# Optimization experiments

Hardware: AMD Instinct MI355X
Metric: run time of the kernel (lower is better)

## Reference

```python
import jax, jax.numpy as jnp
import numpy as np


def gcn_conv(x, src, dst, W, b, n_nodes):
    """PyG-style GCNConv: add self-loops, symmetric deg^-1/2 normalization,
    linear transform, scatter-add aggregation to dst, then bias."""
    loop = jnp.arange(n_nodes, dtype=src.dtype)
    s = jnp.concatenate([src, loop])
    d = jnp.concatenate([dst, loop])
    deg = jax.ops.segment_sum(jnp.ones_like(d, x.dtype), d, num_segments=n_nodes)
    dinv = jax.lax.rsqrt(deg)  # deg >= 1 due to self-loops
    norm = dinv[s] * dinv[d]  # [E+N]
    h = x @ W.T  # [N, out]
    msg = h[s] * norm[:, None]  # [E+N, out]
    return jax.ops.segment_sum(msg, d, num_segments=n_nodes) + b


def setup_inputs() -> dict:
    key = jax.random.key(0)
    k = jax.random.split(key, 6)
    N, E, IN, HID, OUT = 100000, 1600000, 128, 128, 64
    x = jax.random.normal(k[0], (N, IN), dtype=jnp.float32)
    edge_index = jax.random.randint(k[1], (2, E), 0, N, dtype=jnp.int64)
    W1 = jax.random.normal(k[2], (HID, IN), dtype=jnp.float32) * 0.05
    b1 = jnp.zeros((HID,), dtype=jnp.float32)
    W2 = jax.random.normal(k[3], (OUT, HID), dtype=jnp.float32) * 0.05
    b2 = jnp.zeros((OUT,), dtype=jnp.float32)
    return {"x": x, "W1": W1, "b1": b1, "W2": W2, "b2": b2, "edge_index": edge_index}


def reference(x, W1, b1, W2, b2, edge_index):
    n_nodes = x.shape[0]
    src, dst = edge_index[0], edge_index[1]
    h = jax.nn.relu(gcn_conv(x, src, dst, W1, b1, n_nodes))
    return gcn_conv(h, src, dst, W2, b2, n_nodes)
```

## Files before the change

### kernel.cpp

```cpp
#include <hip/hip_runtime.h>
#include <hip/hip_bf16.h>


#define IN_F  128
#define HID_F 128
#define OUT_F 64

#define NPB     512
#define MAXBKT  256
#define CHUNK   4096
#define SLAB    12288
#define CAP     12288

typedef __bf16 bf16_t;
typedef __bf16 bf16x4 __attribute__((ext_vector_type(4)));
typedef __bf16 bf16x8 __attribute__((ext_vector_type(8)));
typedef float  f32x2  __attribute__((ext_vector_type(2)));
typedef float  f32x4  __attribute__((ext_vector_type(4)));
typedef unsigned u32x2 __attribute__((ext_vector_type(2)));
typedef unsigned u32x4 __attribute__((ext_vector_type(4)));

__global__ __launch_bounds__(256) void k_pre(const float* __restrict__ W1s,
                                             const float* __restrict__ W2s,
                                             bf16_t* __restrict__ Wdst,
                                             int n1, int n2,
                                             int* __restrict__ bcur, int nb16) {
    int i = blockIdx.x * 256 + threadIdx.x;
    if (i < n1) Wdst[i] = (bf16_t)W1s[i];
    else if (i < n1 + n2) Wdst[i] = (bf16_t)W2s[i - n1];
    if (blockIdx.x == gridDim.x - 1) {
        for (int j = threadIdx.x; j < nb16; j += 256) bcur[j] = 0;
    }
}

__global__ __launch_bounds__(256) void k_part(const int* __restrict__ src,
                                              const int* __restrict__ dst, int E,
                                              int* __restrict__ bcur,
                                              unsigned* __restrict__ part, int NBKT) {
    __shared__ int cnt[MAXBKT];
    __shared__ int base[MAXBKT];
    __shared__ int cstart[MAXBKT];
    __shared__ unsigned stg[CHUNK];
    __shared__ unsigned short sbk[CHUNK];
    int t = threadIdx.x;
    cnt[t] = 0;
    __syncthreads();
    int cbase = blockIdx.x * CHUNK;
    int cend = min(cbase + CHUNK, E);
    int clen = cend - cbase;
    for (int e = cbase + t; e < cend; e += 256)
        atomicAdd(&cnt[dst[e] >> 9], 1);
    __syncthreads();
    int c = cnt[t];
    cstart[t] = c;
    __syncthreads();
    for (int ofs = 1; ofs < 256; ofs <<= 1) {
        int add = (t >= ofs) ? cstart[t - ofs] : 0;
        __syncthreads();
        cstart[t] += add;
        __syncthreads();
    }
    int excl = cstart[t] - c;
    __syncthreads();
    cstart[t] = excl;
    base[t] = (c && t < NBKT) ? (t * SLAB + atomicAdd(&bcur[t * 16], c)) : 0;
    cnt[t] = 0;
    __syncthreads();
    for (int e = cbase + t; e < cend; e += 256) {
        int d = dst[e];
        int b = d >> 9;
        int lp = atomicAdd(&cnt[b], 1);
        int pos = cstart[b] + lp;
        stg[pos] = (unsigned)src[e] | ((unsigned)(d & 511) << 17);
        sbk[pos] = (unsigned short)b;
    }
    __syncthreads();
    for (int i = t; i < clen; i += 256) {
        int b = sbk[i];
        part[base[b] + (i - cstart[b])] = stg[i];
    }
}

__global__ __launch_bounds__(512) void k_bucket(const unsigned* __restrict__ part,
                                                const int* __restrict__ bcur,
                                                int2* __restrict__ off2,
                                                int* __restrict__ col,
                                                float* __restrict__ dinv, int N) {
    __shared__ int lcnt[NPB];
    __shared__ int lexc[NPB];
    __shared__ int lcur[NPB];
    __shared__ int psum[NPB];
    __shared__ int stage[CAP];
    int b = blockIdx.x;
    int t = threadIdx.x;
    int node0 = b * NPB;
    int e0s = b * SLAB;
    int cnt = bcur[b * 16];
    lcnt[t] = 0;
    __syncthreads();
    for (int i = t; i < cnt; i += 512)
        atomicAdd(&lcnt[part[e0s + i] >> 17], 1);
    __syncthreads();
    int pc = (lcnt[t] + 7) & ~7;
    psum[t] = pc;
    __syncthreads();
    for (int ofs = 1; ofs < NPB; ofs <<= 1) {
        int add = (t >= ofs) ? psum[t - ofs] : 0;
        __syncthreads();
        psum[t] += add;
        __syncthreads();
    }
    int run = psum[t] - pc;
    lexc[t] = run;
    lcur[t] = run;
    int node = node0 + t;
    if (node < N) {
        off2[node] = make_int2(e0s + run, e0s + run + pc);
        dinv[node] = rsqrtf((float)lcnt[t] + 1.0f);
    }
    __syncthreads();
    for (int i = t; i < cnt; i += 512) {
        unsigned p = part[e0s + i];
        int dl = p >> 17;
        int sv = (int)(p & 0x1FFFF);
        int lp = atomicAdd(&lcur[dl], 1);
        if (lp < CAP) stage[lp] = sv;
        else col[e0s + lp] = sv;
    }
    __syncthreads();
    {
        int en = lexc[t] + pc;
        for (int i = lcur[t]; i < en; i++) {
            if (i < CAP) stage[i] = N; else col[e0s + i] = N;
        }
    }
    __syncthreads();
    int tot = psum[NPB - 1];
    for (int i = t; i < tot && i < CAP; i += 512) col[e0s + i] = stage[i];
}

template <int NCOL, typename TIN>
__global__ __launch_bounds__(256) void k_gemm_mfma(const TIN* __restrict__ X,
                                                   const bf16_t* __restrict__ W,
                                                   const float* __restrict__ scale,
                                                   bf16_t* __restrict__ H, int N) {
    constexpr int CT = NCOL / 16;
    int wv = threadIdx.x >> 6, lane = threadIdx.x & 63;
    int quad = lane >> 4, l16 = lane & 15;
    int row0 = blockIdx.x * 128 + wv * 32;
    f32x4 acc[2][CT] = {};
#pragma unroll
    for (int ks = 0; ks < 4; ks++) {
        int k0 = ks * 32 + quad * 8;
        bf16x8 a[2];
#pragma unroll
        for (int rt = 0; rt < 2; rt++) {
            int r = row0 + rt * 16 + l16;
            if (r >= N) r = N - 1;
            const TIN* p = X + (size_t)r * 128 + k0;
            if constexpr (sizeof(TIN) == 4) {
                f32x4 x0 = *(const f32x4*)p;
                f32x4 x1 = *(const f32x4*)(p + 4);
                bf16x8 tt;
                tt[0] = (bf16_t)x0[0]; tt[1] = (bf16_t)x0[1];
                tt[2] = (bf16_t)x0[2]; tt[3] = (bf16_t)x0[3];
                tt[4] = (bf16_t)x1[0]; tt[5] = (bf16_t)x1[1];
                tt[6] = (bf16_t)x1[2]; tt[7] = (bf16_t)x1[3];
                a[rt] = tt;
            } else {
                a[rt] = *(const bf16x8*)p;
            }
        }
#pragma unroll
        for (int ct = 0; ct < CT; ct++) {
            bf16x8 bfrag = *(const bf16x8*)(W + (size_t)(ct * 16 + l16) * 128 + k0);
#pragma unroll
            for (int rt = 0; rt < 2; rt++)
                acc[rt][ct] = __builtin_amdgcn_mfma_f32_16x16x32_bf16(a[rt], bfrag, acc[rt][ct], 0, 0, 0);
        }
    }
#pragma unroll
    for (int rt = 0; rt < 2; rt++)
#pragma unroll
        for (int r4 = 0; r4 < 4; r4++) {
            int r = row0 + rt * 16 + quad * 4 + r4;
            if (r < N) {
                float sc = scale[r];
#pragma unroll
                for (int ct = 0; ct < CT; ct++)
                    H[(size_t)r * NCOL + ct * 16 + l16] = (bf16_t)(sc * acc[rt][ct][r4]);
            } else if (r == N) {
#pragma unroll
                for (int ct = 0; ct < CT; ct++)
                    H[(size_t)N * NCOL + ct * 16 + l16] = (bf16_t)0.f;
            }
        }
}

template <int ROWE>
__device__ __forceinline__ void gather8(const bf16_t* __restrict__ hp,
                                        const int* __restrict__ col, int e,
                                        u32x4* w) {
    int4 c0 = *(const int4*)(col + e);
    int4 c1 = *(const int4*)(col + e + 4);
    w[0] = *(const u32x4*)(hp + (unsigned)c0.x * (unsigned)ROWE);
    w[1] = *(const u32x4*)(hp + (unsigned)c0.y * (unsigned)ROWE);
    w[2] = *(const u32x4*)(hp + (unsigned)c0.z * (unsigned)ROWE);
    w[3] = *(const u32x4*)(hp + (unsigned)c0.w * (unsigned)ROWE);
    w[4] = *(const u32x4*)(hp + (unsigned)c1.x * (unsigned)ROWE);
    w[5] = *(const u32x4*)(hp + (unsigned)c1.y * (unsigned)ROWE);
    w[6] = *(const u32x4*)(hp + (unsigned)c1.z * (unsigned)ROWE);
    w[7] = *(const u32x4*)(hp + (unsigned)c1.w * (unsigned)ROWE);
}

__device__ __forceinline__ void accum8(const u32x4* w, f32x2* a2) {
#pragma unroll
    for (int u = 0; u < 8; u++)
#pragma unroll
        for (int k = 0; k < 4; k++) {
            f32x2 v;
            v.x = __uint_as_float(w[u][k] << 16);
            v.y = __uint_as_float(w[u][k] & 0xffff0000u);
            a2[k] += v;
        }
}

__global__ __launch_bounds__(256) void k_agg_gemm(const bf16_t* __restrict__ h,
                                                  const int2* __restrict__ off2,
                                                  const int* __restrict__ col,
                                                  const float* __restrict__ dinv,
                                                  const float* __restrict__ bias,
                                                  const bf16_t* __restrict__ W2,
                                                  bf16_t* __restrict__ h2, int N) {
    __shared__ float hl[16][132];
    __shared__ float dl[16];
    int lane = threadIdx.x & 63;
    int wv = threadIdx.x >> 6;
    int g = lane >> 4, fl = lane & 15;
    int node0 = blockIdx.x * 16;
    int node = node0 + wv * 4 + g;
    bool alive = node < N;
    int f = fl * 8;
    const bf16_t* hp = h + f;
    f32x2 a2[4] = {};
    float di = 0.f;
    if (alive) {
        u32x4 ws = *(const u32x4*)(hp + (unsigned)node * 128u);
        int2 oe = off2[node];
        di = dinv[node];
#pragma unroll
        for (int k = 0; k < 4; k++) {
            f32x2 v;
            v.x = __uint_as_float(ws[k] << 16);
            v.y = __uint_as_float(ws[k] & 0xffff0000u);
            a2[k] = v;
        }
        u32x4 w[8];
        for (int e = oe.x; e < oe.y; e += 8) {
            gather8<128>(hp, col, e, w);
            accum8(w, a2);
        }
    }
    f32x4 b0 = *(const f32x4*)(bias + f);
    f32x4 b1 = *(const f32x4*)(bias + f + 4);
    int lr = wv * 4 + g;
#pragma unroll
    for (int j = 0; j < 8; j++) {
        float bv = (j < 4) ? b0[j] : b1[j - 4];
        float val = a2[j >> 1][j & 1] * di + bv;
        hl[lr][f + j] = fmaxf(val, 0.f);
    }
    if (fl == 0) dl[lr] = di;
    __syncthreads();

    int quad = lane >> 4, l16 = lane & 15;
    f32x4 c4 = {0.f, 0.f, 0.f, 0.f};
#pragma unroll
    for (int ks = 0; ks < 4; ks++) {
        int k0 = ks * 32 + quad * 8;
        bf16x8 afr;
#pragma unroll
        for (int j = 0; j < 8; j++) afr[j] = (bf16_t)hl[l16][k0 + j];
        bf16x8 bfr = *(const bf16x8*)(W2 + (size_t)(wv * 16 + l16) * 128 + k0);
        c4 = __builtin_amdgcn_mfma_f32_16x16x32_bf16(afr, bfr, c4, 0, 0, 0);
    }
#pragma unroll
    for (int r4 = 0; r4 < 4; r4++) {
        int rr = quad * 4 + r4;
        int gn = node0 + rr;
        if (gn < N)
            h2[(size_t)gn * 64 + wv * 16 + l16] = (bf16_t)(dl[rr] * c4[r4]);
    }
    if (blockIdx.x == 0 && threadIdx.x < 32)
        ((unsigned*)h2)[(size_t)N * 32 + threadIdx.x] = 0u;
}

template <int ROWE, int LPN, bool RELU, typename TOUT>
__global__ __launch_bounds__(256) void k_agg(const bf16_t* __restrict__ h,
                                             const int2* __restrict__ off2,
                                             const int* __restrict__ col,
                                             const float* __restrict__ dinv,
                                             const float* __restrict__ bias,
                                             TOUT* __restrict__ out, int N) {
    constexpr int NPW = 64 / LPN;
    int lane = threadIdx.x & 63;
    int wv = threadIdx.x >> 6;
    int g = lane / LPN, fl = lane % LPN;
    int node = blockIdx.x * (4 * NPW) + wv * NPW + g;
    if (node >= N) return;
    int f = fl * 8;
    const bf16_t* hp = h + f;
    u32x4 ws = *(const u32x4*)(hp + (unsigned)node * (unsigned)ROWE);
    int2 oe = off2[node];
    float di = dinv[node];
    f32x2 a2[4];
#pragma unroll
    for (int k = 0; k < 4; k++) {
        f32x2 v;
        v.x = __uint_as_float(ws[k] << 16);
        v.y = __uint_as_float(ws[k] & 0xffff0000u);
        a2[k] = v;
    }
    u32x4 w[8];
    for (int e = oe.x; e < oe.y; e += 8) {
        gather8<ROWE>(hp, col, e, w);
        accum8(w, a2);
    }
    f32x4 b0 = *(const f32x4*)(bias + f);
    f32x4 b1 = *(const f32x4*)(bias + f + 4);
    float r[8];
#pragma unroll
    for (int j = 0; j < 8; j++) {
        float bv = (j < 4) ? b0[j] : b1[j - 4];
        float val = a2[j >> 1][j & 1] * di + bv;
        if (RELU) val = fmaxf(val, 0.f);
        r[j] = val;
    }
    if constexpr (sizeof(TOUT) == 2) {
        bf16x8 v;
#pragma unroll
        for (int j = 0; j < 8; j++) v[j] = (bf16_t)r[j];
        *(bf16x8*)((bf16_t*)out + (size_t)node * ROWE + f) = v;
    } else {
        f32x4 v0 = {r[0], r[1], r[2], r[3]};
        f32x4 v1 = {r[4], r[5], r[6], r[7]};
        *(f32x4*)((float*)out + (size_t)node * ROWE + f) = v0;
        *(f32x4*)((float*)out + (size_t)node * ROWE + f + 4) = v1;
    }
}

extern "C" void kernel_launch(void* const* d_in, const int* in_sizes, int n_in,
                              void* d_out, int out_size, void* d_ws, size_t ws_size,
                              hipStream_t stream) {
    const float* x  = (const float*)d_in[0];
    const float* W1 = (const float*)d_in[1];
    const float* b1 = (const float*)d_in[2];
    const float* W2 = (const float*)d_in[3];
    const float* b2 = (const float*)d_in[4];
    const int*   ei = (const int*)d_in[5];

    int N = in_sizes[0] / IN_F;
    int E = in_sizes[5] / 2;
    const int* src = ei;
    const int* dst = ei + E;
    int NBKT = (N + NPB - 1) / NPB;
    int pchunks = (E + CHUNK - 1) / CHUNK;

    size_t woff = 0;
    auto alloc = [&](size_t bytes) {
        void* p = (char*)d_ws + woff;
        woff += (bytes + 255) & ~(size_t)255;
        return p;
    };
    int*      bcur  = (int*)alloc((size_t)NBKT * 16 * 4);
    unsigned* part  = (unsigned*)alloc((size_t)NBKT * SLAB * 4);
    int*      col   = (int*)alloc((size_t)NBKT * SLAB * 4);
    int2*     off2  = (int2*)alloc((size_t)N * 8);
    float*    dinv  = (float*)alloc((size_t)N * 4);
    bf16_t*   Wb    = (bf16_t*)alloc((size_t)(HID_F * IN_F + OUT_F * HID_F) * 2);
    bf16_t*   W1b   = Wb;
    bf16_t*   W2b   = Wb + HID_F * IN_F;
    bf16_t*   h1    = (bf16_t*)alloc((size_t)(N + 1) * HID_F * 2);
    bf16_t*   h2b   = (bf16_t*)alloc((size_t)(N + 1) * OUT_F * 2);
    float*    outp  = (float*)d_out;

    int n1 = HID_F * IN_F, n2 = OUT_F * HID_F;
    int preblocks = (n1 + n2) / 256 + 1;
    k_pre<<<preblocks, 256, 0, stream>>>(W1, W2, Wb, n1, n2, bcur, NBKT * 16);
    k_part<<<pchunks, 256, 0, stream>>>(src, dst, E, bcur, part, NBKT);
    k_bucket<<<NBKT, 512, 0, stream>>>(part, bcur, off2, col, dinv, N);

    int gemm_blocks = (N + 127) / 128;

    k_gemm_mfma<HID_F, float><<<gemm_blocks, 256, 0, stream>>>(x, W1b, dinv, h1, N);
    k_agg_gemm<<<(N + 15) / 16, 256, 0, stream>>>(h1, off2, col, dinv, b1, W2b, h2b, N);
    k_agg<OUT_F, 8, false, float><<<(N + 31) / 32, 256, 0, stream>>>(h2b, off2, col, dinv, b2, outp, N);
}
```

Baseline: 251.9 us.

## Merge preprocessing kernels, compute degrees via global atomics, overlap GEMM with bucketing

The weight conversion now runs inside the partition kernel as extra blocks. The partition kernel also counts in-degrees with global atomics, so the first GEMM no longer waits for per-bucket CSR construction. The GEMM is launched as extra blocks of the bucket kernel so the two run side by side, and bucket entries are kept in registers between the counting and scatter passes. The aim is fewer launches and less serial dependency, paid for with 1.6M global atomics on deg, a memset, and rsqrt recomputed in each consumer.

```diff
diff --git a/kernel.cpp b/kernel.cpp
--- a/kernel.cpp
+++ b/kernel.cpp
@@ -11,45 +11,46 @@
 #define CHUNK   4096
 #define SLAB    12288
 #define CAP     12288
+#define KREG    20
 
 typedef __bf16 bf16_t;
-typedef __bf16 bf16x4 __attribute__((ext_vector_type(4)));
 typedef __bf16 bf16x8 __attribute__((ext_vector_type(8)));
 typedef float  f32x2  __attribute__((ext_vector_type(2)));
 typedef float  f32x4  __attribute__((ext_vector_type(4)));
-typedef unsigned u32x2 __attribute__((ext_vector_type(2)));
 typedef unsigned u32x4 __attribute__((ext_vector_type(4)));
 
-__global__ __launch_bounds__(256) void k_pre(const float* __restrict__ W1s,
-                                             const float* __restrict__ W2s,
-                                             bf16_t* __restrict__ Wdst,
-                                             int n1, int n2,
-                                             int* __restrict__ bcur, int nb16) {
-    int i = blockIdx.x * 256 + threadIdx.x;
-    if (i < n1) Wdst[i] = (bf16_t)W1s[i];
-    else if (i < n1 + n2) Wdst[i] = (bf16_t)W2s[i - n1];
-    if (blockIdx.x == gridDim.x - 1) {
-        for (int j = threadIdx.x; j < nb16; j += 256) bcur[j] = 0;
-    }
-}
-
-__global__ __launch_bounds__(256) void k_part(const int* __restrict__ src,
-                                              const int* __restrict__ dst, int E,
-                                              int* __restrict__ bcur,
-                                              unsigned* __restrict__ part, int NBKT) {
+__global__ __launch_bounds__(256) void k_setup(const int* __restrict__ src,
+                                               const int* __restrict__ dst, int E,
+                                               int* __restrict__ bcur,
+                                               unsigned* __restrict__ part,
+                                               int* __restrict__ deg,
+                                               const float* __restrict__ W1s,
+                                               const float* __restrict__ W2s,
+                                               bf16_t* __restrict__ Wdst,
+                                               int n1, int n2,
+                                               int NBKT, int pchunks) {
+    int t = threadIdx.x;
+    if ((int)blockIdx.x >= pchunks) {
+        int i = (blockIdx.x - pchunks) * 256 + t;
+        if (i < n1) Wdst[i] = (bf16_t)W1s[i];
+        else if (i < n1 + n2) Wdst[i] = (bf16_t)W2s[i - n1];
+        return;
+    }
     __shared__ int cnt[MAXBKT];
     __shared__ int base[MAXBKT];
     __shared__ int cstart[MAXBKT];
     __shared__ unsigned stg[CHUNK];
     __shared__ unsigned short sbk[CHUNK];
-    int t = threadIdx.x;
     cnt[t] = 0;
     __syncthreads();
     int cbase = blockIdx.x * CHUNK;
     int cend = min(cbase + CHUNK, E);
     int clen = cend - cbase;
-    for (int e = cbase + t; e < cend; e += 256)
-        atomicAdd(&cnt[dst[e] >> 9], 1);
+    for (int e = cbase + t; e < cend; e += 256) {
+        int d = dst[e];
+        atomicAdd(&cnt[d >> 9], 1);
+        atomicAdd(&deg[d], 1);
+    }
     __syncthreads();
     int c = cnt[t];
     cstart[t] = c;
@@ -81,84 +82,36 @@
     }
 }
 
-__global__ __launch_bounds__(512) void k_bucket(const unsigned* __restrict__ part,
-                                                const int* __restrict__ bcur,
-                                                int2* __restrict__ off2,
-                                                int* __restrict__ col,
-                                                float* __restrict__ dinv, int N) {
+__global__ __launch_bounds__(512) void k_mega2(const unsigned* __restrict__ part,
+                                               const int* __restrict__ bcur,
+                                               int2* __restrict__ off2,
+                                               int* __restrict__ col,
+                                               const int* __restrict__ deg,
+                                               const float* __restrict__ X,
+                                               const bf16_t* __restrict__ W1,
+                                               bf16_t* __restrict__ H,
+                                               int N, int NBKT) {
     __shared__ int lcnt[NPB];
     __shared__ int lexc[NPB];
     __shared__ int lcur[NPB];
     __shared__ int psum[NPB];
     __shared__ int stage[CAP];
-    int b = blockIdx.x;
     int t = threadIdx.x;
-    int node0 = b * NPB;
-    int e0s = b * SLAB;
-    int cnt = bcur[b * 16];
-    lcnt[t] = 0;
-    __syncthreads();
-    for (int i = t; i < cnt; i += 512)
-        atomicAdd(&lcnt[part[e0s + i] >> 17], 1);
-    __syncthreads();
-    int pc = (lcnt[t] + 7) & ~7;
-    psum[t] = pc;
-    __syncthreads();
-    for (int ofs = 1; ofs < NPB; ofs <<= 1) {
-        int add = (t >= ofs) ? psum[t - ofs] : 0;
-        __syncthreads();
-        psum[t] += add;
-        __syncthreads();
-    }
-    int run = psum[t] - pc;
-    lexc[t] = run;
-    lcur[t] = run;
-    int node = node0 + t;
-    if (node < N) {
-        off2[node] = make_int2(e0s + run, e0s + run + pc);
-        dinv[node] = rsqrtf((float)lcnt[t] + 1.0f);
-    }
-    __syncthreads();
-    for (int i = t; i < cnt; i += 512) {
-        unsigned p = part[e0s + i];
-        int dl = p >> 17;
-        int sv = (int)(p & 0x1FFFF);
-        int lp = atomicAdd(&lcur[dl], 1);
-        if (lp < CAP) stage[lp] = sv;
-        else col[e0s + lp] = sv;
-    }
-    __syncthreads();
-    {
-        int en = lexc[t] + pc;
-        for (int i = lcur[t]; i < en; i++) {
-            if (i < CAP) stage[i] = N; else col[e0s + i] = N;
-        }
-    }
-    __syncthreads();
-    int tot = psum[NPB - 1];
-    for (int i = t; i < tot && i < CAP; i += 512) col[e0s + i] = stage[i];
-}
-
-template <int NCOL, typename TIN>
-__global__ __launch_bounds__(256) void k_gemm_mfma(const TIN* __restrict__ X,
-                                                   const bf16_t* __restrict__ W,
-                                                   const float* __restrict__ scale,
-                                                   bf16_t* __restrict__ H, int N) {
-    constexpr int CT = NCOL / 16;
-    int wv = threadIdx.x >> 6, lane = threadIdx.x & 63;
-    int quad = lane >> 4, l16 = lane & 15;
-    int row0 = blockIdx.x * 128 + wv * 32;
-    f32x4 acc[2][CT] = {};
-#pragma unroll
-    for (int ks = 0; ks < 4; ks++) {
-        int k0 = ks * 32 + quad * 8;
-        bf16x8 a[2];
-#pragma unroll
-        for (int rt = 0; rt < 2; rt++) {
-            int r = row0 + rt * 16 + l16;
-            if (r >= N) r = N - 1;
-            const TIN* p = X + (size_t)r * 128 + k0;
-            if constexpr (sizeof(TIN) == 4) {
+    if ((int)blockIdx.x >= NBKT) {
+        int gb = blockIdx.x - NBKT;
+        int wv = t >> 6, lane = t & 63;
+        int quad = lane >> 4, l16 = lane & 15;
+        int row0 = gb * 256 + wv * 32;
+        f32x4 acc[2][8] = {};
+#pragma unroll
+        for (int ks = 0; ks < 4; ks++) {
+            int k0 = ks * 32 + quad * 8;
+            bf16x8 a[2];
+#pragma unroll
+            for (int rt = 0; rt < 2; rt++) {
+                int r = row0 + rt * 16 + l16;
+                if (r >= N) r = N - 1;
+                const float* p = X + (size_t)r * 128 + k0;
                 f32x4 x0 = *(const f32x4*)p;
                 f32x4 x1 = *(const f32x4*)(p + 4);
                 bf16x8 tt;
@@ -167,34 +120,98 @@
                 tt[4] = (bf16_t)x1[0]; tt[5] = (bf16_t)x1[1];
                 tt[6] = (bf16_t)x1[2]; tt[7] = (bf16_t)x1[3];
                 a[rt] = tt;
-            } else {
-                a[rt] = *(const bf16x8*)p;
             }
-        }
-#pragma unroll
-        for (int ct = 0; ct < CT; ct++) {
-            bf16x8 bfrag = *(const bf16x8*)(W + (size_t)(ct * 16 + l16) * 128 + k0);
-#pragma unroll
-            for (int rt = 0; rt < 2; rt++)
-                acc[rt][ct] = __builtin_amdgcn_mfma_f32_16x16x32_bf16(a[rt], bfrag, acc[rt][ct], 0, 0, 0);
-        }
-    }
-#pragma unroll
-    for (int rt = 0; rt < 2; rt++)
-#pragma unroll
-        for (int r4 = 0; r4 < 4; r4++) {
-            int r = row0 + rt * 16 + quad * 4 + r4;
-            if (r < N) {
-                float sc = scale[r];
-#pragma unroll
-                for (int ct = 0; ct < CT; ct++)
-                    H[(size_t)r * NCOL + ct * 16 + l16] = (bf16_t)(sc * acc[rt][ct][r4]);
-            } else if (r == N) {
-#pragma unroll
-                for (int ct = 0; ct < CT; ct++)
-                    H[(size_t)N * NCOL + ct * 16 + l16] = (bf16_t)0.f;
+#pragma unroll
+            for (int ct = 0; ct < 8; ct++) {
+                bf16x8 bfrag = *(const bf16x8*)(W1 + (size_t)(ct * 16 + l16) * 128 + k0);
+#pragma unroll
+                for (int rt = 0; rt < 2; rt++)
+                    acc[rt][ct] = __builtin_amdgcn_mfma_f32_16x16x32_bf16(a[rt], bfrag, acc[rt][ct], 0, 0, 0);
             }
         }
+#pragma unroll
+        for (int rt = 0; rt < 2; rt++)
+#pragma unroll
+            for (int r4 = 0; r4 < 4; r4++) {
+                int r = row0 + rt * 16 + quad * 4 + r4;
+                if (r < N) {
+                    float sc = rsqrtf((float)deg[r] + 1.0f);
+#pragma unroll
+                    for (int ct = 0; ct < 8; ct++)
+                        H[(size_t)r * 128 + ct * 16 + l16] = (bf16_t)(sc * acc[rt][ct][r4]);
+                } else if (r == N) {
+#pragma unroll
+                    for (int ct = 0; ct < 8; ct++)
+                        H[(size_t)N * 128 + ct * 16 + l16] = (bf16_t)0.f;
+                }
+            }
+        return;
+    }
+    int b = blockIdx.x;
+    int node0 = b * NPB;
+    int e0s = b * SLAB;
+    int cnt = bcur[b * 16];
+    lcnt[t] = 0;
+    __syncthreads();
+    unsigned rv[KREG];
+    int nk = (cnt + 511) >> 9;
+#pragma unroll
+    for (int k = 0; k < KREG; k++) {
+        int i = k * 512 + t;
+        if (k < nk && i < cnt) {
+            rv[k] = part[e0s + i];
+            atomicAdd(&lcnt[rv[k] >> 17], 1);
+        }
+    }
+    for (int i = KREG * 512 + t; i < cnt; i += 512)
+        atomicAdd(&lcnt[part[e0s + i] >> 17], 1);
+    __syncthreads();
+    int pc = (lcnt[t] + 7) & ~7;
+    psum[t] = pc;
+    __syncthreads();
+    for (int ofs = 1; ofs < NPB; ofs <<= 1) {
+        int add = (t >= ofs) ? psum[t - ofs] : 0;
+        __syncthreads();
+        psum[t] += add;
+        __syncthreads();
+    }
+    int run = psum[t] - pc;
+    lexc[t] = run;
+    lcur[t] = run;
+    int node = node0 + t;
+    if (node < N)
+        off2[node] = make_int2(e0s + run, e0s + run + pc);
+    __syncthreads();
+#pragma unroll
+    for (int k = 0; k < KREG; k++) {
+        int i = k * 512 + t;
+        if (k < nk && i < cnt) {
+            unsigned p = rv[k];
+            int dl = p >> 17;
+            int sv = (int)(p & 0x1FFFF);
+            int lp = atomicAdd(&lcur[dl], 1);
+            if (lp < CAP) stage[lp] = sv;
+            else col[e0s + lp] = sv;
+        }
+    }
+    for (int i = KREG * 512 + t; i < cnt; i += 512) {
+        unsigned p = part[e0s + i];
+        int dl = p >> 17;
+        int sv = (int)(p & 0x1FFFF);
+        int lp = atomicAdd(&lcur[dl], 1);
+        if (lp < CAP) stage[lp] = sv;
+        else col[e0s + lp] = sv;
+    }
+    __syncthreads();
+    {
+        int en = lexc[t] + pc;
+        for (int i = lcur[t]; i < en; i++) {
+            if (i < CAP) stage[i] = N; else col[e0s + i] = N;
+        }
+    }
+    __syncthreads();
+    int tot = psum[NPB - 1];
+    for (int i = t; i < tot && i < CAP; i += 512) col[e0s + i] = stage[i];
 }
 
 template <int ROWE>
@@ -228,7 +245,7 @@
 __global__ __launch_bounds__(256) void k_agg_gemm(const bf16_t* __restrict__ h,
                                                   const int2* __restrict__ off2,
                                                   const int* __restrict__ col,
-                                                  const float* __restrict__ dinv,
+                                                  const int* __restrict__ deg,
                                                   const float* __restrict__ bias,
                                                   const bf16_t* __restrict__ W2,
                                                   bf16_t* __restrict__ h2, int N) {
@@ -247,7 +264,7 @@
     if (alive) {
         u32x4 ws = *(const u32x4*)(hp + (unsigned)node * 128u);
         int2 oe = off2[node];
-        di = dinv[node];
+        di = rsqrtf((float)deg[node] + 1.0f);
 #pragma unroll
         for (int k = 0; k < 4; k++) {
             f32x2 v;
@@ -299,7 +316,7 @@
 __global__ __launch_bounds__(256) void k_agg(const bf16_t* __restrict__ h,
                                              const int2* __restrict__ off2,
                                              const int* __restrict__ col,
-                                             const float* __restrict__ dinv,
+                                             const int* __restrict__ deg,
                                              const float* __restrict__ bias,
                                              TOUT* __restrict__ out, int N) {
     constexpr int NPW = 64 / LPN;
@@ -312,7 +329,7 @@
     const bf16_t* hp = h + f;
     u32x4 ws = *(const u32x4*)(hp + (unsigned)node * (unsigned)ROWE);
     int2 oe = off2[node];
-    float di = dinv[node];
+    float di = rsqrtf((float)deg[node] + 1.0f);
     f32x2 a2[4];
 #pragma unroll
     for (int k = 0; k < 4; k++) {
@@ -373,10 +390,10 @@
         return p;
     };
     int*      bcur  = (int*)alloc((size_t)NBKT * 16 * 4);
+    int*      deg   = (int*)alloc((size_t)N * 4);
     unsigned* part  = (unsigned*)alloc((size_t)NBKT * SLAB * 4);
     int*      col   = (int*)alloc((size_t)NBKT * SLAB * 4);
     int2*     off2  = (int2*)alloc((size_t)N * 8);
-    float*    dinv  = (float*)alloc((size_t)N * 4);
     bf16_t*   Wb    = (bf16_t*)alloc((size_t)(HID_F * IN_F + OUT_F * HID_F) * 2);
     bf16_t*   W1b   = Wb;
     bf16_t*   W2b   = Wb + HID_F * IN_F;
@@ -384,15 +401,19 @@
     bf16_t*   h2b   = (bf16_t*)alloc((size_t)(N + 1) * OUT_F * 2);
     float*    outp  = (float*)d_out;
 
+    size_t zbytes = (size_t)((char*)deg - (char*)bcur) + (size_t)N * 4;
+    hipMemsetAsync(bcur, 0, zbytes, stream);
+
     int n1 = HID_F * IN_F, n2 = OUT_F * HID_F;
-    int preblocks = (n1 + n2) / 256 + 1;
-    k_pre<<<preblocks, 256, 0, stream>>>(W1, W2, Wb, n1, n2, bcur, NBKT * 16);
-    k_part<<<pchunks, 256, 0, stream>>>(src, dst, E, bcur, part, NBKT);
-    k_bucket<<<NBKT, 512, 0, stream>>>(part, bcur, off2, col, dinv, N);
-
-    int gemm_blocks = (N + 127) / 128;
-
-    k_gemm_mfma<HID_F, float><<<gemm_blocks, 256, 0, stream>>>(x, W1b, dinv, h1, N);
-    k_agg_gemm<<<(N + 15) / 16, 256, 0, stream>>>(h1, off2, col, dinv, b1, W2b, h2b, N);
-    k_agg<OUT_F, 8, false, float><<<(N + 31) / 32, 256, 0, stream>>>(h2b, off2, col, dinv, b2, outp, N);
-}
+    int wconvblocks = (n1 + n2 + 255) / 256;
+    k_setup<<<pchunks + wconvblocks, 256, 0, stream>>>(src, dst, E, bcur, part, deg,
+                                                       W1, W2, Wb, n1, n2,
+                                                       NBKT, pchunks);
+
+    int gemmblocks = (N + 255) / 256;
+    k_mega2<<<NBKT + gemmblocks, 512, 0, stream>>>(part, bcur, off2, col, deg,
+                                                   x, W1b, h1, N, NBKT);
+
+    k_agg_gemm<<<(N + 15) / 16, 256, 0, stream>>>(h1, off2, col, deg, b1, W2b, h2b, N);
+    k_agg<OUT_F, 8, false, float><<<(N + 31) / 32, 256, 0, stream>>>(h2b, off2, col, deg, b2, outp, N);
+}
```

Result: slower. 302.3 us (+20.0%).

## Fuse first-layer GEMM into bucket CSR build with smaller node buckets

Applied to the files above, without the earlier changes.

Merges the first-layer MFMA GEMM into the bucket kernel, so each block builds CSR for its 256 nodes and then computes the scaled X·W1 rows for those same nodes, reading dinv from shared memory. This removes one kernel launch and the global dinv reload. Buckets shrink from 512 to 256 nodes, which doubles the bucket count, and the partition kernel now handles 512 bucket counters with two per thread. The cost is a GEMM tail serialized behind the CSR build inside each block, plus higher shared-memory atomic traffic in the partition kernel.

```diff
diff --git a/kernel.cpp b/kernel.cpp
--- a/kernel.cpp
+++ b/kernel.cpp
@@ -6,18 +6,16 @@
 #define HID_F 128
 #define OUT_F 64
 
-#define NPB     512
-#define MAXBKT  256
+#define NPB     256
+#define MAXBKT  512
 #define CHUNK   4096
-#define SLAB    12288
-#define CAP     12288
+#define SLAB    6144
+#define CAP     6144
 
 typedef __bf16 bf16_t;
-typedef __bf16 bf16x4 __attribute__((ext_vector_type(4)));
 typedef __bf16 bf16x8 __attribute__((ext_vector_type(8)));
 typedef float  f32x2  __attribute__((ext_vector_type(2)));
 typedef float  f32x4  __attribute__((ext_vector_type(4)));
-typedef unsigned u32x2 __attribute__((ext_vector_type(2)));
 typedef unsigned u32x4 __attribute__((ext_vector_type(4)));
 
 __global__ __launch_bounds__(256) void k_pre(const float* __restrict__ W1s,
@@ -40,38 +38,40 @@
     __shared__ int cnt[MAXBKT];
     __shared__ int base[MAXBKT];
     __shared__ int cstart[MAXBKT];
+    __shared__ int psum[256];
     __shared__ unsigned stg[CHUNK];
     __shared__ unsigned short sbk[CHUNK];
     int t = threadIdx.x;
-    cnt[t] = 0;
+    cnt[t] = 0; cnt[t + 256] = 0;
     __syncthreads();
     int cbase = blockIdx.x * CHUNK;
     int cend = min(cbase + CHUNK, E);
     int clen = cend - cbase;
     for (int e = cbase + t; e < cend; e += 256)
-        atomicAdd(&cnt[dst[e] >> 9], 1);
-    __syncthreads();
-    int c = cnt[t];
-    cstart[t] = c;
+        atomicAdd(&cnt[dst[e] >> 8], 1);
+    __syncthreads();
+    int c0 = cnt[2 * t], c1 = cnt[2 * t + 1];
+    psum[t] = c0 + c1;
     __syncthreads();
     for (int ofs = 1; ofs < 256; ofs <<= 1) {
-        int add = (t >= ofs) ? cstart[t - ofs] : 0;
+        int add = (t >= ofs) ? psum[t - ofs] : 0;
         __syncthreads();
-        cstart[t] += add;
+        psum[t] += add;
         __syncthreads();
     }
-    int excl = cstart[t] - c;
-    __syncthreads();
-    cstart[t] = excl;
-    base[t] = (c && t < NBKT) ? (t * SLAB + atomicAdd(&bcur[t * 16], c)) : 0;
-    cnt[t] = 0;
+    int ex = psum[t] - (c0 + c1);
+    cstart[2 * t] = ex;
+    cstart[2 * t + 1] = ex + c0;
+    base[2 * t] = (c0 && 2 * t < NBKT) ? (2 * t * SLAB + atomicAdd(&bcur[2 * t * 16], c0)) : 0;
+    base[2 * t + 1] = (c1 && 2 * t + 1 < NBKT) ? ((2 * t + 1) * SLAB + atomicAdd(&bcur[(2 * t + 1) * 16], c1)) : 0;
+    cnt[2 * t] = 0; cnt[2 * t + 1] = 0;
     __syncthreads();
     for (int e = cbase + t; e < cend; e += 256) {
         int d = dst[e];
-        int b = d >> 9;
+        int b = d >> 8;
         int lp = atomicAdd(&cnt[b], 1);
         int pos = cstart[b] + lp;
-        stg[pos] = (unsigned)src[e] | ((unsigned)(d & 511) << 17);
+        stg[pos] = (unsigned)src[e] | ((unsigned)(d & 255) << 17);
         sbk[pos] = (unsigned short)b;
     }
     __syncthreads();
@@ -81,15 +81,20 @@
     }
 }
 
-__global__ __launch_bounds__(512) void k_bucket(const unsigned* __restrict__ part,
-                                                const int* __restrict__ bcur,
-                                                int2* __restrict__ off2,
-                                                int* __restrict__ col,
-                                                float* __restrict__ dinv, int N) {
+__global__ __launch_bounds__(256) void k_bucket_gemm(const unsigned* __restrict__ part,
+                                                     const int* __restrict__ bcur,
+                                                     int2* __restrict__ off2,
+                                                     int* __restrict__ col,
+                                                     float* __restrict__ dinv,
+                                                     const float* __restrict__ X,
+                                                     const bf16_t* __restrict__ W1,
+                                                     bf16_t* __restrict__ H,
+                                                     int N) {
     __shared__ int lcnt[NPB];
     __shared__ int lexc[NPB];
     __shared__ int lcur[NPB];
     __shared__ int psum[NPB];
+    __shared__ float dinvl[NPB];
     __shared__ int stage[CAP];
     int b = blockIdx.x;
     int t = threadIdx.x;
@@ -98,7 +103,7 @@
     int cnt = bcur[b * 16];
     lcnt[t] = 0;
     __syncthreads();
-    for (int i = t; i < cnt; i += 512)
+    for (int i = t; i < cnt; i += 256)
         atomicAdd(&lcnt[part[e0s + i] >> 17], 1);
     __syncthreads();
     int pc = (lcnt[t] + 7) & ~7;
@@ -113,13 +118,15 @@
     int run = psum[t] - pc;
     lexc[t] = run;
     lcur[t] = run;
+    float di = rsqrtf((float)lcnt[t] + 1.0f);
+    dinvl[t] = di;
     int node = node0 + t;
     if (node < N) {
         off2[node] = make_int2(e0s + run, e0s + run + pc);
-        dinv[node] = rsqrtf((float)lcnt[t] + 1.0f);
-    }
-    __syncthreads();
-    for (int i = t; i < cnt; i += 512) {
+        dinv[node] = di;
+    }
+    __syncthreads();
+    for (int i = t; i < cnt; i += 256) {
         unsigned p = part[e0s + i];
         int dl = p >> 17;
         int sv = (int)(p & 0x1FFFF);
@@ -136,29 +143,23 @@
     }
     __syncthreads();
     int tot = psum[NPB - 1];
-    for (int i = t; i < tot && i < CAP; i += 512) col[e0s + i] = stage[i];
-}
-
-template <int NCOL, typename TIN>
-__global__ __launch_bounds__(256) void k_gemm_mfma(const TIN* __restrict__ X,
-                                                   const bf16_t* __restrict__ W,
-                                                   const float* __restrict__ scale,
-                                                   bf16_t* __restrict__ H, int N) {
-    constexpr int CT = NCOL / 16;
-    int wv = threadIdx.x >> 6, lane = threadIdx.x & 63;
+    for (int i = t; i < tot && i < CAP; i += 256) col[e0s + i] = stage[i];
+
+    int wv = t >> 6, lane = t & 63;
     int quad = lane >> 4, l16 = lane & 15;
-    int row0 = blockIdx.x * 128 + wv * 32;
-    f32x4 acc[2][CT] = {};
-#pragma unroll
-    for (int ks = 0; ks < 4; ks++) {
-        int k0 = ks * 32 + quad * 8;
-        bf16x8 a[2];
-#pragma unroll
-        for (int rt = 0; rt < 2; rt++) {
-            int r = row0 + rt * 16 + l16;
-            if (r >= N) r = N - 1;
-            const TIN* p = X + (size_t)r * 128 + k0;
-            if constexpr (sizeof(TIN) == 4) {
+#pragma unroll
+    for (int rh = 0; rh < 2; rh++) {
+        int row0 = node0 + rh * 128 + wv * 32;
+        f32x4 acc[2][8] = {};
+#pragma unroll
+        for (int ks = 0; ks < 4; ks++) {
+            int k0 = ks * 32 + quad * 8;
+            bf16x8 a[2];
+#pragma unroll
+            for (int rt = 0; rt < 2; rt++) {
+                int r = row0 + rt * 16 + l16;
+                if (r >= N) r = N - 1;
+                const float* p = X + (size_t)r * 128 + k0;
                 f32x4 x0 = *(const f32x4*)p;
                 f32x4 x1 = *(const f32x4*)(p + 4);
                 bf16x8 tt;
@@ -167,34 +168,32 @@
                 tt[4] = (bf16_t)x1[0]; tt[5] = (bf16_t)x1[1];
                 tt[6] = (bf16_t)x1[2]; tt[7] = (bf16_t)x1[3];
                 a[rt] = tt;
-            } else {
-                a[rt] = *(const bf16x8*)p;
             }
-        }
-#pragma unroll
-        for (int ct = 0; ct < CT; ct++) {
-            bf16x8 bfrag = *(const bf16x8*)(W + (size_t)(ct * 16 + l16) * 128 + k0);
-#pragma unroll
-            for (int rt = 0; rt < 2; rt++)
-                acc[rt][ct] = __builtin_amdgcn_mfma_f32_16x16x32_bf16(a[rt], bfrag, acc[rt][ct], 0, 0, 0);
-        }
-    }
-#pragma unroll
-    for (int rt = 0; rt < 2; rt++)
-#pragma unroll
-        for (int r4 = 0; r4 < 4; r4++) {
-            int r = row0 + rt * 16 + quad * 4 + r4;
-            if (r < N) {
-                float sc = scale[r];
-#pragma unroll
-                for (int ct = 0; ct < CT; ct++)
-                    H[(size_t)r * NCOL + ct * 16 + l16] = (bf16_t)(sc * acc[rt][ct][r4]);
-            } else if (r == N) {
-#pragma unroll
-                for (int ct = 0; ct < CT; ct++)
-                    H[(size_t)N * NCOL + ct * 16 + l16] = (bf16_t)0.f;
+#pragma unroll
+            for (int ct = 0; ct < 8; ct++) {
+                bf16x8 bfrag = *(const bf16x8*)(W1 + (size_t)(ct * 16 + l16) * 128 + k0);
+#pragma unroll
+                for (int rt = 0; rt < 2; rt++)
+                    acc[rt][ct] = __builtin_amdgcn_mfma_f32_16x16x32_bf16(a[rt], bfrag, acc[rt][ct], 0, 0, 0);
             }
         }
+#pragma unroll
+        for (int rt = 0; rt < 2; rt++)
+#pragma unroll
+            for (int r4 = 0; r4 < 4; r4++) {
+                int r = row0 + rt * 16 + quad * 4 + r4;
+                if (r < N) {
+                    float sc = dinvl[r - node0];
+#pragma unroll
+                    for (int ct = 0; ct < 8; ct++)
+                        H[(size_t)r * 128 + ct * 16 + l16] = (bf16_t)(sc * acc[rt][ct][r4]);
+                } else if (r == N) {
+#pragma unroll
+                    for (int ct = 0; ct < 8; ct++)
+                        H[(size_t)N * 128 + ct * 16 + l16] = (bf16_t)0.f;
+                }
+            }
+    }
 }
 
 template <int ROWE>
@@ -388,11 +387,8 @@
     int preblocks = (n1 + n2) / 256 + 1;
     k_pre<<<preblocks, 256, 0, stream>>>(W1, W2, Wb, n1, n2, bcur, NBKT * 16);
     k_part<<<pchunks, 256, 0, stream>>>(src, dst, E, bcur, part, NBKT);
-    k_bucket<<<NBKT, 512, 0, stream>>>(part, bcur, off2, col, dinv, N);
-
-    int gemm_blocks = (N + 127) / 128;
-
-    k_gemm_mfma<HID_F, float><<<gemm_blocks, 256, 0, stream>>>(x, W1b, dinv, h1, N);
+    k_bucket_gemm<<<NBKT, 256, 0, stream>>>(part, bcur, off2, col, dinv,
+                                            x, W1b, h1, N);
     k_agg_gemm<<<(N + 15) / 16, 256, 0, stream>>>(h1, off2, col, dinv, b1, W2b, h2b, N);
     k_agg<OUT_F, 8, false, float><<<(N + 31) / 32, 256, 0, stream>>>(h2b, off2, col, dinv, b2, outp, N);
 }
```

New measurement: 253.7 us. Within noise of the previous version (+0.7%).
